# Performance work log

Measured on AMD Instinct MI355X. Metric: run time of the kernel, lower is better.

Reference implementation:

```python
import jax, jax.numpy as jnp
import numpy as np

CODEBOOK_SIZE = 1024
LATENT_CHANNELS = 256
COMMIT_LOSS_BETA = 0.25


def setup_inputs() -> dict:
    key = jax.random.key(0)
    k1, k2 = jax.random.split(key)
    inputs = jax.random.normal(k1, (32, LATENT_CHANNELS, 32, 32), dtype=jnp.float32)
    bound = 1.0 / CODEBOOK_SIZE
    codebook_w = jax.random.uniform(
        k2, (CODEBOOK_SIZE, LATENT_CHANNELS), dtype=jnp.float32,
        minval=-bound, maxval=bound)
    return {"inputs": inputs, "codebook_w": codebook_w}


def reference(inputs, codebook_w):
    # NCHW -> NHWC, flatten spatial+batch to tokens
    x = jnp.transpose(inputs, (0, 2, 3, 1))          # [B,H,W,C]
    flat = x.reshape(-1, LATENT_CHANNELS)            # [N,C]

    dists = (jnp.sum(flat ** 2, axis=1, keepdims=True)
             - 2.0 * (flat @ codebook_w.T)
             + jnp.sum(codebook_w ** 2, axis=1))
    code_idxs = jnp.argmin(dists, axis=1)            # [N]

    quantized = codebook_w[code_idxs].reshape(x.shape)  # [B,H,W,C]

    # use_ema=False branch: embedding loss pulls codebook toward (detached) inputs
    embedding_loss = jnp.mean((quantized - jax.lax.stop_gradient(x)) ** 2)
    commitment_loss = jnp.mean((jax.lax.stop_gradient(quantized) - x) ** 2)
    vq_loss = commitment_loss * COMMIT_LOSS_BETA + embedding_loss

    # straight-through estimator
    quantized_st = x + jax.lax.stop_gradient(quantized - x)
    out = jnp.transpose(quantized_st, (0, 3, 1, 2))  # back to NCHW
    return out, vq_loss, embedding_loss, commitment_loss
```

## Files before the change

kernel.cpp:

```cpp
#include <hip/hip_runtime.h>
#include <cfloat>

typedef short bf16x8 __attribute__((ext_vector_type(8)));
typedef float f32x4  __attribute__((ext_vector_type(4)));

#define NCH 16

static __device__ __forceinline__ void gl_lds16(const void* g, void* l) {
    __builtin_amdgcn_global_load_lds(
        (const __attribute__((address_space(1))) unsigned int*)g,
        (__attribute__((address_space(3))) unsigned int*)l, 16, 0, 0);
}

__global__ __launch_bounds__(256) void prep_kernel(
    const float* __restrict__ W, unsigned short* __restrict__ wh,
    float* __restrict__ cw, float* __restrict__ lossAcc)
{
    int t   = threadIdx.x;
    int row = blockIdx.x * 16 + (t >> 4);
    int c0  = (t & 15) * 16;
    const float* wr = W + row * 256 + c0;
    float s = 0.f;
    unsigned int packed[8];
#pragma unroll
    for (int i = 0; i < 16; i += 2) {
        float a = wr[i], b = wr[i + 1];
        s += a * a + b * b;
        unsigned short ha = __builtin_bit_cast(unsigned short, (__bf16)a);
        unsigned short hb = __builtin_bit_cast(unsigned short, (__bf16)b);
        packed[i >> 1] = (unsigned int)ha | ((unsigned int)hb << 16);
    }
    uint4* dst = (uint4*)&wh[row * 256 + c0];
    dst[0] = make_uint4(packed[0], packed[1], packed[2], packed[3]);
    dst[1] = make_uint4(packed[4], packed[5], packed[6], packed[7]);
#pragma unroll
    for (int m = 1; m < 16; m <<= 1) s += __shfl_xor(s, m, 64);
    if ((t & 15) == 0) cw[row] = s;
    if (blockIdx.x == 0 && t == 0) *lossAcc = 0.f;
}

__global__ __launch_bounds__(256, 2) void argmin_kernel(
    const float* __restrict__ X, const unsigned short* __restrict__ wh,
    const float* __restrict__ cw, int* __restrict__ gidx,
    float* __restrict__ lossAcc)
{
    __shared__ unsigned short whs[2][4][16 * 256];

    int tid  = threadIdx.x;
    int lane = tid & 63;
    int q    = tid >> 6;
    int srow = lane & 15;
    int kgrp = lane >> 4;
    int b    = blockIdx.x;
    int batch = b >> 4;
    int sbase = (b & 15) * 64;
    const float* xb = X + ((size_t)batch << 18) + sbase;

    const char* whb = (const char*)wh;
    int rl0 = lane >> 5;
    int gcol = lane & 31;

    auto stage = [&](int ch, int buf) {
        char* ldsbase = (char*)&whs[buf][q][0];
        int codeBase = q * 256 + ch * 16;
#pragma unroll
        for (int c = 0; c < 8; ++c) {
            int r  = c * 2 + rl0;
            int gs = gcol ^ (r & 7);
            gl_lds16(whb + (size_t)(codeBase + r) * 512 + gs * 16, ldsbase + c * 1024);
        }
    };

    stage(0, 0);

    bf16x8 fx[4][8];
    float tpart[4] = {0.f, 0.f, 0.f, 0.f};
#pragma unroll
    for (int tt = 0; tt < 4; ++tt) {
#pragma unroll
        for (int ks = 0; ks < 8; ++ks) {
            bf16x8 h;
#pragma unroll
            for (int i = 0; i < 8; ++i) {
                int c = ks * 32 + kgrp * 8 + i;
                float v = xb[((size_t)c << 10) + tt * 16 + srow];
                h[i] = (short)__builtin_bit_cast(unsigned short, (__bf16)v);
                tpart[tt] = fmaf(v, v, tpart[tt]);
            }
            fx[tt][ks] = h;
        }
        tpart[tt] += __shfl_xor(tpart[tt], 16, 64);
        tpart[tt] += __shfl_xor(tpart[tt], 32, 64);
    }

    asm volatile("s_waitcnt vmcnt(0)" ::: "memory");

    float best[4] = {FLT_MAX, FLT_MAX, FLT_MAX, FLT_MAX};
    int   bidx[4] = {0, 0, 0, 0};
    const float* cwq = cw + q * 256;
    int cur = 0;

    for (int ch = 0; ch < NCH; ++ch) {
        if (ch + 1 < NCH) stage(ch + 1, cur ^ 1);
        float4 cw4 = *(const float4*)&cwq[ch * 16 + kgrp * 4];

        const unsigned short* wq = &whs[cur][q][0];
        bf16x8 af[8];
#pragma unroll
        for (int ks = 0; ks < 8; ++ks)
            af[ks] = *(const bf16x8*)&wq[srow * 256 + (((ks * 4 + kgrp) ^ (srow & 7)) * 8)];

        f32x4 acc[4];
#pragma unroll
        for (int tt = 0; tt < 4; ++tt) acc[tt] = (f32x4){0.f, 0.f, 0.f, 0.f};
#pragma unroll
        for (int ks = 0; ks < 8; ++ks)
#pragma unroll
            for (int tt = 0; tt < 4; ++tt)
                acc[tt] = __builtin_amdgcn_mfma_f32_16x16x32_bf16(
                    af[ks], fx[tt][ks], acc[tt], 0, 0, 0);

        int cb = q * 256 + ch * 16 + kgrp * 4;
#pragma unroll
        for (int j = 0; j < 4; ++j) {
            float cwv = j == 0 ? cw4.x : j == 1 ? cw4.y : j == 2 ? cw4.z : cw4.w;
#pragma unroll
            for (int tt = 0; tt < 4; ++tt) {
                float e = fmaf(-2.f, acc[tt][j], cwv);
                bool better = e < best[tt];
                best[tt] = better ? e : best[tt];
                bidx[tt] = better ? (cb + j) : bidx[tt];
            }
        }
        asm volatile("s_waitcnt vmcnt(0)" ::: "memory");
        cur ^= 1;
    }

    __syncthreads();
    float* redv = (float*)&whs[0][0][0];
    int*   redi = (int*)((char*)&whs[0][0][0] + 1024);
    float* redt = (float*)((char*)&whs[0][0][0] + 2048);

#pragma unroll
    for (int tt = 0; tt < 4; ++tt) {
        float v = best[tt]; int id = bidx[tt];
#pragma unroll
        for (int m = 16; m <= 32; m <<= 1) {
            float ve = __shfl_xor(v, m, 64);
            int   ie = __shfl_xor(id, m, 64);
            if (ve < v || (ve == v && ie < id)) { v = ve; id = ie; }
        }
        if (lane < 16) {
            redv[q * 64 + tt * 16 + lane] = v;
            redi[q * 64 + tt * 16 + lane] = id;
            if (q == 0) redt[tt * 16 + lane] = tpart[tt];
        }
    }
    __syncthreads();

    if (tid < 64) {
        float v = redv[tid]; int id = redi[tid];
#pragma unroll
        for (int qq = 1; qq < 4; ++qq) {
            float vq = redv[qq * 64 + tid];
            if (vq < v) { v = vq; id = redi[qq * 64 + tid]; }
        }
        gidx[b * 64 + tid] = id;
        float dl = redt[tid] + v;
#pragma unroll
        for (int m = 1; m < 64; m <<= 1) dl += __shfl_xor(dl, m, 64);
        if (tid == 0) atomicAdd(lossAcc, dl);
    }
}

__global__ __launch_bounds__(256) void out_kernel(
    const float* __restrict__ W, const int* __restrict__ gidx,
    const float* __restrict__ lossAcc, float* __restrict__ out)
{
    __shared__ float tile[256][65];
    __shared__ int lidx[64];
    int t = threadIdx.x, g = blockIdx.x;
    int n0 = g * 64;
    int b = n0 >> 10, sb = n0 & 1023;
    if (t < 64) lidx[t] = gidx[n0 + t];
    __syncthreads();
    int tok = t >> 2, cq = t & 3;
    const float* wr = W + ((size_t)lidx[tok] << 8);
#pragma unroll
    for (int j = 0; j < 16; ++j) {
        int c = cq * 4 + j * 16;
        float4 v = *(const float4*)&wr[c];
        tile[c + 0][tok] = v.x; tile[c + 1][tok] = v.y;
        tile[c + 2][tok] = v.z; tile[c + 3][tok] = v.w;
    }
    __syncthreads();
    float* op = out + (((size_t)(b * 256 + t)) << 10) + sb;
#pragma unroll
    for (int j = 0; j < 16; ++j) {
        float4 v;
        v.x = tile[t][j * 4 + 0]; v.y = tile[t][j * 4 + 1];
        v.z = tile[t][j * 4 + 2]; v.w = tile[t][j * 4 + 3];
        *(float4*)&op[j * 4] = v;
    }
    if (g == 0 && t == 0) {
        float mse = *lossAcc * (1.0f / 8388608.0f);
        out[8388608] = 1.25f * mse;
        out[8388609] = mse;
        out[8388610] = mse;
    }
}

extern "C" void kernel_launch(void* const* d_in, const int* in_sizes, int n_in,
                              void* d_out, int out_size, void* d_ws, size_t ws_size,
                              hipStream_t stream)
{
    (void)in_sizes; (void)n_in; (void)out_size; (void)ws_size;
    const float* X = (const float*)d_in[0];
    const float* W = (const float*)d_in[1];
    float* out = (float*)d_out;
    char* ws = (char*)d_ws;
    float*          lossAcc = (float*)ws;
    float*          cw      = (float*)(ws + 256);
    unsigned short* wh      = (unsigned short*)(ws + 256 + 4096);
    int*            gidx    = (int*)(ws + 256 + 4096 + 524288);

    prep_kernel<<<64, 256, 0, stream>>>(W, wh, cw, lossAcc);
    argmin_kernel<<<512, 256, 0, stream>>>(X, wh, cw, gidx, lossAcc);
    out_kernel<<<512, 256, 0, stream>>>(W, gidx, lossAcc, out);
}
```

Before: 54.17 us.

## Pretranspose inputs to bf16 tokens and keep codebook quarter resident in LDS

The prep kernel now also converts X from NCHW to a token-major, swizzled bf16 buffer and computes each token's squared norm. The argmin kernel uses 512-thread blocks that load a full 256-code quarter of the codebook into LDS once, so 512 tokens reuse it, replacing the per-block double-buffered streaming. Per-quarter partial minima are written out, and the final cross-quarter reduction, loss accumulation and a last-block counter finalization move into the output kernel. This trades an extra round trip of a bf16 copy of X through memory and a 128KB LDS footprint, which limits occupancy, for less redundant codebook traffic and strided X reads in the hot loop.

```diff
diff --git a/kernel.cpp b/kernel.cpp
--- a/kernel.cpp
+++ b/kernel.cpp
@@ -3,8 +3,6 @@
 
 typedef short bf16x8 __attribute__((ext_vector_type(8)));
 typedef float f32x4  __attribute__((ext_vector_type(4)));
-
-#define NCH 16
 
 static __device__ __forceinline__ void gl_lds16(const void* g, void* l) {
     __builtin_amdgcn_global_load_lds(
@@ -12,103 +10,104 @@
         (__attribute__((address_space(3))) unsigned int*)l, 16, 0, 0);
 }
 
+static __device__ __forceinline__ unsigned int pack2(float a, float b) {
+    unsigned short ha = __builtin_bit_cast(unsigned short, (__bf16)a);
+    unsigned short hb = __builtin_bit_cast(unsigned short, (__bf16)b);
+    return (unsigned int)ha | ((unsigned int)hb << 16);
+}
+
 __global__ __launch_bounds__(256) void prep_kernel(
-    const float* __restrict__ W, unsigned short* __restrict__ wh,
-    float* __restrict__ cw, float* __restrict__ lossAcc)
-{
-    int t   = threadIdx.x;
-    int row = blockIdx.x * 16 + (t >> 4);
-    int c0  = (t & 15) * 16;
-    const float* wr = W + row * 256 + c0;
-    float s = 0.f;
-    unsigned int packed[8];
-#pragma unroll
-    for (int i = 0; i < 16; i += 2) {
-        float a = wr[i], b = wr[i + 1];
-        s += a * a + b * b;
-        unsigned short ha = __builtin_bit_cast(unsigned short, (__bf16)a);
-        unsigned short hb = __builtin_bit_cast(unsigned short, (__bf16)b);
-        packed[i >> 1] = (unsigned int)ha | ((unsigned int)hb << 16);
-    }
-    uint4* dst = (uint4*)&wh[row * 256 + c0];
-    dst[0] = make_uint4(packed[0], packed[1], packed[2], packed[3]);
-    dst[1] = make_uint4(packed[4], packed[5], packed[6], packed[7]);
-#pragma unroll
-    for (int m = 1; m < 16; m <<= 1) s += __shfl_xor(s, m, 64);
-    if ((t & 15) == 0) cw[row] = s;
-    if (blockIdx.x == 0 && t == 0) *lossAcc = 0.f;
-}
-
-__global__ __launch_bounds__(256, 2) void argmin_kernel(
-    const float* __restrict__ X, const unsigned short* __restrict__ wh,
-    const float* __restrict__ cw, int* __restrict__ gidx,
-    float* __restrict__ lossAcc)
-{
-    __shared__ unsigned short whs[2][4][16 * 256];
-
+    const float* __restrict__ W, const float* __restrict__ X,
+    unsigned short* __restrict__ wh, float* __restrict__ cw,
+    unsigned short* __restrict__ xt, float* __restrict__ xnorm,
+    float* __restrict__ lossAcc, unsigned int* __restrict__ counter)
+{
+    int t = threadIdx.x, blk = blockIdx.x;
+    if (blk < 64) {
+        int row = blk * 16 + (t >> 4);
+        int c0  = (t & 15) * 16;
+        const float* wr = W + row * 256 + c0;
+        float s = 0.f;
+        unsigned int pk[8];
+#pragma unroll
+        for (int i = 0; i < 16; i += 2) {
+            float a = wr[i], b = wr[i + 1];
+            s += a * a + b * b;
+            pk[i >> 1] = pack2(a, b);
+        }
+        int g0 = (t & 15) * 2, e = row & 7;
+        uint4* dst = (uint4*)&wh[row * 256];
+        dst[g0 ^ e]       = make_uint4(pk[0], pk[1], pk[2], pk[3]);
+        dst[(g0 + 1) ^ e] = make_uint4(pk[4], pk[5], pk[6], pk[7]);
+#pragma unroll
+        for (int m = 1; m < 16; m <<= 1) s += __shfl_xor(s, m, 64);
+        if ((t & 15) == 0) cw[row] = s;
+        if (blk == 0 && t == 0) { *lossAcc = 0.f; *counter = 0u; }
+    } else {
+        int tok = (blk - 64) * 256 + t;
+        int b = tok >> 10, s = tok & 1023;
+        const float* xp = X + ((size_t)b << 18) + s;
+        float acc = 0.f;
+        int e = tok & 7;
+        uint4* dst = (uint4*)&xt[(size_t)tok * 256];
+#pragma unroll
+        for (int g = 0; g < 32; ++g) {
+            unsigned int pk[4];
+#pragma unroll
+            for (int p = 0; p < 4; ++p) {
+                float a = xp[(size_t)(g * 8 + p * 2)     << 10];
+                float c = xp[(size_t)(g * 8 + p * 2 + 1) << 10];
+                acc = fmaf(a, a, fmaf(c, c, acc));
+                pk[p] = pack2(a, c);
+            }
+            dst[g ^ e] = make_uint4(pk[0], pk[1], pk[2], pk[3]);
+        }
+        xnorm[tok] = acc;
+    }
+}
+
+__global__ __launch_bounds__(512, 2) void argmin_kernel(
+    const unsigned short* __restrict__ wh, const unsigned short* __restrict__ xt,
+    const float* __restrict__ cw, float2* __restrict__ partial)
+{
+    __shared__ unsigned short wlds[256 * 256];
     int tid  = threadIdx.x;
-    int lane = tid & 63;
-    int q    = tid >> 6;
-    int srow = lane & 15;
-    int kgrp = lane >> 4;
-    int b    = blockIdx.x;
-    int batch = b >> 4;
-    int sbase = (b & 15) * 64;
-    const float* xb = X + ((size_t)batch << 18) + sbase;
-
-    const char* whb = (const char*)wh;
-    int rl0 = lane >> 5;
-    int gcol = lane & 31;
-
-    auto stage = [&](int ch, int buf) {
-        char* ldsbase = (char*)&whs[buf][q][0];
-        int codeBase = q * 256 + ch * 16;
-#pragma unroll
-        for (int c = 0; c < 8; ++c) {
-            int r  = c * 2 + rl0;
-            int gs = gcol ^ (r & 7);
-            gl_lds16(whb + (size_t)(codeBase + r) * 512 + gs * 16, ldsbase + c * 1024);
-        }
-    };
-
-    stage(0, 0);
-
+    int lane = tid & 63, w = tid >> 6;
+    int g = blockIdx.x >> 2, q = blockIdx.x & 3;
+    int srow = lane & 15, kgrp = lane >> 4;
+
+    const char* wsrc = (const char*)wh + (size_t)(q * 256 + w * 32) * 512;
+    char* wdst = (char*)wlds + w * 16384;
+#pragma unroll
+    for (int j = 0; j < 16; ++j)
+        gl_lds16(wsrc + j * 1024 + lane * 16, wdst + j * 1024);
+
+    int T0 = g * 512 + w * 64;
     bf16x8 fx[4][8];
-    float tpart[4] = {0.f, 0.f, 0.f, 0.f};
 #pragma unroll
     for (int tt = 0; tt < 4; ++tt) {
-#pragma unroll
-        for (int ks = 0; ks < 8; ++ks) {
-            bf16x8 h;
-#pragma unroll
-            for (int i = 0; i < 8; ++i) {
-                int c = ks * 32 + kgrp * 8 + i;
-                float v = xb[((size_t)c << 10) + tt * 16 + srow];
-                h[i] = (short)__builtin_bit_cast(unsigned short, (__bf16)v);
-                tpart[tt] = fmaf(v, v, tpart[tt]);
-            }
-            fx[tt][ks] = h;
-        }
-        tpart[tt] += __shfl_xor(tpart[tt], 16, 64);
-        tpart[tt] += __shfl_xor(tpart[tt], 32, 64);
-    }
-
+        int T = T0 + tt * 16 + srow, e = T & 7;
+        const unsigned short* xr = xt + (size_t)T * 256;
+#pragma unroll
+        for (int ks = 0; ks < 8; ++ks)
+            fx[tt][ks] = *(const bf16x8*)&xr[((ks * 4 + kgrp) ^ e) * 8];
+    }
     asm volatile("s_waitcnt vmcnt(0)" ::: "memory");
+    __syncthreads();
 
     float best[4] = {FLT_MAX, FLT_MAX, FLT_MAX, FLT_MAX};
     int   bidx[4] = {0, 0, 0, 0};
     const float* cwq = cw + q * 256;
-    int cur = 0;
-
-    for (int ch = 0; ch < NCH; ++ch) {
-        if (ch + 1 < NCH) stage(ch + 1, cur ^ 1);
+
+    for (int ch = 0; ch < 16; ++ch) {
+        int r = ch * 16 + srow, eb = r & 7;
+        const unsigned short* ar = &wlds[r * 256];
+        bf16x8 af[8];
+#pragma unroll
+        for (int ks = 0; ks < 8; ++ks)
+            af[ks] = *(const bf16x8*)&ar[((ks * 4 + kgrp) ^ eb) * 8];
+
         float4 cw4 = *(const float4*)&cwq[ch * 16 + kgrp * 4];
-
-        const unsigned short* wq = &whs[cur][q][0];
-        bf16x8 af[8];
-#pragma unroll
-        for (int ks = 0; ks < 8; ++ks)
-            af[ks] = *(const bf16x8*)&wq[srow * 256 + (((ks * 4 + kgrp) ^ (srow & 7)) * 8)];
 
         f32x4 acc[4];
 #pragma unroll
@@ -126,20 +125,13 @@
             float cwv = j == 0 ? cw4.x : j == 1 ? cw4.y : j == 2 ? cw4.z : cw4.w;
 #pragma unroll
             for (int tt = 0; tt < 4; ++tt) {
-                float e = fmaf(-2.f, acc[tt][j], cwv);
-                bool better = e < best[tt];
-                best[tt] = better ? e : best[tt];
+                float e2 = fmaf(-2.f, acc[tt][j], cwv);
+                bool better = e2 < best[tt];
+                best[tt] = better ? e2 : best[tt];
                 bidx[tt] = better ? (cb + j) : bidx[tt];
             }
         }
-        asm volatile("s_waitcnt vmcnt(0)" ::: "memory");
-        cur ^= 1;
-    }
-
-    __syncthreads();
-    float* redv = (float*)&whs[0][0][0];
-    int*   redi = (int*)((char*)&whs[0][0][0] + 1024);
-    float* redt = (float*)((char*)&whs[0][0][0] + 2048);
+    }
 
 #pragma unroll
     for (int tt = 0; tt < 4; ++tt) {
@@ -150,40 +142,50 @@
             int   ie = __shfl_xor(id, m, 64);
             if (ve < v || (ve == v && ie < id)) { v = ve; id = ie; }
         }
-        if (lane < 16) {
-            redv[q * 64 + tt * 16 + lane] = v;
-            redi[q * 64 + tt * 16 + lane] = id;
-            if (q == 0) redt[tt * 16 + lane] = tpart[tt];
-        }
-    }
-    __syncthreads();
-
-    if (tid < 64) {
-        float v = redv[tid]; int id = redi[tid];
-#pragma unroll
-        for (int qq = 1; qq < 4; ++qq) {
-            float vq = redv[qq * 64 + tid];
-            if (vq < v) { v = vq; id = redi[qq * 64 + tid]; }
-        }
-        gidx[b * 64 + tid] = id;
-        float dl = redt[tid] + v;
-#pragma unroll
-        for (int m = 1; m < 64; m <<= 1) dl += __shfl_xor(dl, m, 64);
-        if (tid == 0) atomicAdd(lossAcc, dl);
+        if (lane < 16)
+            partial[(size_t)q * 32768 + T0 + tt * 16 + lane] =
+                make_float2(v, __int_as_float(id));
     }
 }
 
 __global__ __launch_bounds__(256) void out_kernel(
-    const float* __restrict__ W, const int* __restrict__ gidx,
-    const float* __restrict__ lossAcc, float* __restrict__ out)
+    const float* __restrict__ W, const float2* __restrict__ partial,
+    const float* __restrict__ xnorm, float* __restrict__ lossAcc,
+    unsigned int* __restrict__ counter, float* __restrict__ out)
 {
     __shared__ float tile[256][65];
     __shared__ int lidx[64];
     int t = threadIdx.x, g = blockIdx.x;
     int n0 = g * 64;
     int b = n0 >> 10, sb = n0 & 1023;
-    if (t < 64) lidx[t] = gidx[n0 + t];
+
+    if (t < 64) {
+        float2 p = partial[n0 + t];
+        float v = p.x; int id = __float_as_int(p.y);
+#pragma unroll
+        for (int q = 1; q < 4; ++q) {
+            float2 pq = partial[(size_t)q * 32768 + n0 + t];
+            if (pq.x < v) { v = pq.x; id = __float_as_int(pq.y); }
+        }
+        lidx[t] = id;
+        float dmin = xnorm[n0 + t] + v;
+#pragma unroll
+        for (int m = 1; m < 64; m <<= 1) dmin += __shfl_xor(dmin, m, 64);
+        if (t == 0) {
+            atomicAdd(lossAcc, dmin);
+            __threadfence();
+            if (atomicAdd(counter, 1u) == 511u) {
+                __threadfence();
+                float tot = atomicAdd(lossAcc, 0.f);
+                float mse = tot * (1.0f / 8388608.0f);
+                out[8388608] = 1.25f * mse;
+                out[8388609] = mse;
+                out[8388610] = mse;
+            }
+        }
+    }
     __syncthreads();
+
     int tok = t >> 2, cq = t & 3;
     const float* wr = W + ((size_t)lidx[tok] << 8);
 #pragma unroll
@@ -201,12 +203,6 @@
         v.x = tile[t][j * 4 + 0]; v.y = tile[t][j * 4 + 1];
         v.z = tile[t][j * 4 + 2]; v.w = tile[t][j * 4 + 3];
         *(float4*)&op[j * 4] = v;
-    }
-    if (g == 0 && t == 0) {
-        float mse = *lossAcc * (1.0f / 8388608.0f);
-        out[8388608] = 1.25f * mse;
-        out[8388609] = mse;
-        out[8388610] = mse;
     }
 }
 
@@ -220,11 +216,14 @@
     float* out = (float*)d_out;
     char* ws = (char*)d_ws;
     float*          lossAcc = (float*)ws;
-    float*          cw      = (float*)(ws + 256);
-    unsigned short* wh      = (unsigned short*)(ws + 256 + 4096);
-    int*            gidx    = (int*)(ws + 256 + 4096 + 524288);
-
-    prep_kernel<<<64, 256, 0, stream>>>(W, wh, cw, lossAcc);
-    argmin_kernel<<<512, 256, 0, stream>>>(X, wh, cw, gidx, lossAcc);
-    out_kernel<<<512, 256, 0, stream>>>(W, gidx, lossAcc, out);
-}
+    unsigned int*   counter = (unsigned int*)(ws + 8);
+    float*          cw      = (float*)(ws + 4096);
+    unsigned short* wh      = (unsigned short*)(ws + 8192);
+    float*          xnorm   = (float*)(ws + 1048576);
+    unsigned short* xt      = (unsigned short*)(ws + 2097152);
+    float2*         partial = (float2*)(ws + 19922944);
+
+    prep_kernel<<<192, 256, 0, stream>>>(W, X, wh, cw, xt, xnorm, lossAcc, counter);
+    argmin_kernel<<<256, 512, 0, stream>>>(wh, xt, cw, partial);
+    out_kernel<<<512, 256, 0, stream>>>(W, partial, xnorm, lossAcc, counter, out);
+}
```

Result: slower. 70.91 us (+30.9%).
